# Optimization experiments

Measured on AMD Instinct MI355X. Metric: run time of the kernel, lower is better.

Reference implementation:

```python
import jax, jax.numpy as jnp
import numpy as np

L, C = 256, 20
BATCH = 1024


def _pairwise_mask(L, C, mask_type='pairwise'):
    # mask[l1, c1, l2, c2] nonzero iff positions interact (l2 - l1 >= 1, or == 1 for neighbor)
    ls = jnp.arange(L)
    d = ls[None, :] - ls[:, None]  # [L, L] = l2 - l1
    m = (d >= 1) if mask_type == 'pairwise' else (d == 1)
    return jnp.broadcast_to(m[:, None, :, None], (L, C, L, C)).astype(jnp.float32)


def setup_inputs() -> dict:
    key = jax.random.key(0)
    k1, k2, k3 = jax.random.split(key, 3)
    x_lc = jax.random.uniform(k1, (BATCH, L * C), dtype=jnp.float32)
    theta_0 = jnp.zeros((1,), dtype=jnp.float32)
    theta_lc = jax.random.normal(k2, (L, C), dtype=jnp.float32) / np.sqrt(L)
    theta_lclc = jax.random.normal(k3, (L, C, L, C), dtype=jnp.float32) / np.sqrt(L * L)
    return {"x_lc": x_lc, "theta_0": theta_0, "theta_lc": theta_lc, "theta_lclc": theta_lclc}


def reference(x_lc, theta_0, theta_lc, theta_lclc):
    Ld, Cd = theta_lc.shape
    mask = _pairwise_mask(Ld, Cd, 'pairwise')
    # additive term: sum_lc theta_lc * x_lc  -> [B, 1]
    lin = x_lc @ theta_lc.reshape(Ld * Cd)  # [B]
    # pairwise term: x^T (theta * mask) x, expressed as a masked GEMM instead of a
    # broadcasted [B, L, C, L, C] product
    Theta = (theta_lclc * mask).reshape(Ld * Cd, Ld * Cd)  # [LC, LC]
    xm = x_lc @ Theta  # [B, LC]
    quad = jnp.sum(xm * x_lc, axis=1)  # [B]
    phi = theta_0 + (lin + quad)[:, None]  # [B, 1]
    return phi
```

## Files before the change

### kernel.cpp

```cpp
#include <hip/hip_runtime.h>
#include <hip/hip_bf16.h>
#include <cstdint>
#include <cstddef>

#define LCN 5120
#define BN  1024
#define CN  20

typedef __attribute__((ext_vector_type(4))) float  floatx4;
typedef __attribute__((ext_vector_type(8))) short  shortx8;
typedef __attribute__((ext_vector_type(4))) unsigned short ushortx4;

static __device__ __forceinline__ unsigned short f2bf(float f) {
    __hip_bfloat16 h = __float2bfloat16(f);
    return *reinterpret_cast<unsigned short*>(&h);
}

static __device__ __forceinline__ void gload_lds16(const void* g, void* l) {
    __builtin_amdgcn_global_load_lds(
        (const __attribute__((address_space(1))) void*)g,
        (__attribute__((address_space(3))) void*)l,
        16, 0, 0);
}

__global__ __launch_bounds__(256) void k_conv(const float* __restrict__ th,
                                              unsigned short* __restrict__ Tn) {
    const int a  = blockIdx.y;
    const int t  = a >> 7;
    const int c0 = (CN * ((128 * t) / CN + 1)) / 512;
    const int bx = blockIdx.x;
    if (2 * (bx + 1) <= c0) return;
    const int kmin = CN * (a / CN + 1);
    const int col  = bx * 1024 + threadIdx.x * 4;
    const floatx4 v = *reinterpret_cast<const floatx4*>(th + (size_t)a * LCN + col);
    ushortx4 o;
#pragma unroll
    for (int e = 0; e < 4; ++e)
        o[e] = (col + e >= kmin) ? f2bf(v[e]) : (unsigned short)0;
    *reinterpret_cast<ushortx4*>(Tn + (size_t)a * LCN + col) = o;
}

__global__ __launch_bounds__(256) void k_init(const float* __restrict__ x,
                                              const float* __restrict__ th0,
                                              const float* __restrict__ thlc,
                                              float* __restrict__ out,
                                              unsigned short* __restrict__ Xb) {
    const int b = blockIdx.x;
    const int tid = threadIdx.x;
    const floatx4* xr = reinterpret_cast<const floatx4*>(x + (size_t)b * LCN);
    const floatx4* tr = reinterpret_cast<const floatx4*>(thlc);
    ushortx4* xw = reinterpret_cast<ushortx4*>(Xb + (size_t)b * LCN);
    float s = 0.0f;
    for (int k = tid; k < LCN / 4; k += 256) {
        const floatx4 a = xr[k], t2 = tr[k];
        s += a[0] * t2[0] + a[1] * t2[1] + a[2] * t2[2] + a[3] * t2[3];
        ushortx4 o;
#pragma unroll
        for (int e = 0; e < 4; ++e) o[e] = f2bf(a[e]);
        xw[k] = o;
    }
#pragma unroll
    for (int off = 32; off > 0; off >>= 1) s += __shfl_down(s, off, 64);
    __shared__ float ws4[4];
    if ((tid & 63) == 0) ws4[tid >> 6] = s;
    __syncthreads();
    if (tid == 0) out[b] = th0[0] + ws4[0] + ws4[1] + ws4[2] + ws4[3];
}

__global__ __launch_bounds__(256) void k_quad(
    const unsigned short* __restrict__ Xb,
    const unsigned short* __restrict__ Tn,
    float*                __restrict__ out,
    const int tot)
{
    const int bid  = blockIdx.x;
    const int xcd  = bid & 7;
    const int slot = bid >> 3;
    const int m    = slot & 7;
    const int g    = slot >> 3;
    int q = g * 8 + xcd;
    if (q >= tot) return;

    __shared__ unsigned short As[2][128 * 32];
    __shared__ unsigned short Bs[2][128 * 32];
    __shared__ float partial[128];

    const int tid  = threadIdx.x;
    const int lane = tid & 63;
    const int w    = tid >> 6;
    const int wm   = w & 1;
    const int wn   = w >> 1;
    const int lrow = lane & 15;
    const int kq   = lane >> 4;

    int n = 0, c = 0;
    for (int t = 0; t < 40; ++t) {
        const int c0t = (CN * ((128 * t) / CN + 1)) / 512;
        const int chn = 10 - c0t;
        if (q < chn) { n = t; c = c0t + q; break; }
        q -= chn;
    }
    const int b0 = m * 128;
    const int n0 = n * 128;
    const int k0 = c * 512;

    if (tid < 128) partial[tid] = 0.0f;

    floatx4 acc[4][4];
#pragma unroll
    for (int mt = 0; mt < 4; ++mt)
#pragma unroll
        for (int nt = 0; nt < 4; ++nt) acc[mt][nt] = (floatx4)0.0f;

    int grow[2], goff[2], loff[2];
#pragma unroll
    for (int t = 0; t < 2; ++t) {
        const int s    = t * 256 + tid;
        const int row  = s >> 2;
        const int gseg = ((s & 3) - (row >> 1)) & 3;
        grow[t] = row;
        goff[t] = gseg * 8;
        loff[t] = (t * 256 + w * 64) * 16;
    }
    int aoff[4], boff[4];
#pragma unroll
    for (int mt = 0; mt < 4; ++mt) {
        const int row = wm * 64 + mt * 16 + lrow;
        aoff[mt] = row * 32 + (((kq + (row >> 1)) & 3) << 3);
    }
#pragma unroll
    for (int nt = 0; nt < 4; ++nt) {
        const int row = wn * 64 + nt * 16 + lrow;
        boff[nt] = row * 32 + (((kq + (row >> 1)) & 3) << 3);
    }

#pragma unroll
    for (int t = 0; t < 2; ++t) {
        gload_lds16(Xb + (size_t)(b0 + grow[t]) * LCN + k0 + goff[t], (char*)As[0] + loff[t]);
        gload_lds16(Tn + (size_t)(n0 + grow[t]) * LCN + k0 + goff[t], (char*)Bs[0] + loff[t]);
    }

    for (int kk = 0; kk < 16; ++kk) {
        const int p = kk & 1;
        __syncthreads();
        if (kk < 15) {
            const int kc = k0 + (kk + 1) * 32;
#pragma unroll
            for (int t = 0; t < 2; ++t) {
                gload_lds16(Xb + (size_t)(b0 + grow[t]) * LCN + kc + goff[t], (char*)As[p ^ 1] + loff[t]);
                gload_lds16(Tn + (size_t)(n0 + grow[t]) * LCN + kc + goff[t], (char*)Bs[p ^ 1] + loff[t]);
            }
        }
        shortx8 af[4], bfr[4];
#pragma unroll
        for (int mt = 0; mt < 4; ++mt)
            af[mt] = *reinterpret_cast<const shortx8*>(As[p] + aoff[mt]);
#pragma unroll
        for (int nt = 0; nt < 4; ++nt)
            bfr[nt] = *reinterpret_cast<const shortx8*>(Bs[p] + boff[nt]);
#pragma unroll
        for (int mt = 0; mt < 4; ++mt)
#pragma unroll
            for (int nt = 0; nt < 4; ++nt)
                acc[mt][nt] = __builtin_amdgcn_mfma_f32_16x16x32_bf16(af[mt], bfr[nt], acc[mt][nt], 0, 0, 0);
    }

#pragma unroll
    for (int mt = 0; mt < 4; ++mt) {
#pragma unroll
        for (int r = 0; r < 4; ++r) {
            const int b = b0 + wm * 64 + mt * 16 + kq * 4 + r;
            float s = 0.0f;
#pragma unroll
            for (int nt = 0; nt < 4; ++nt) {
                const int a = n0 + wn * 64 + nt * 16 + lrow;
                const __hip_bfloat16 hv = *reinterpret_cast<const __hip_bfloat16*>(&Xb[(size_t)b * LCN + a]);
                s += acc[mt][nt][r] * __bfloat162float(hv);
            }
            s += __shfl_xor(s, 1, 64);
            s += __shfl_xor(s, 2, 64);
            s += __shfl_xor(s, 4, 64);
            s += __shfl_xor(s, 8, 64);
            if (lrow == 0) atomicAdd(&partial[b - b0], s);
        }
    }
    __syncthreads();
    if (tid < 128) atomicAdd(&out[b0 + tid], partial[tid]);
}

extern "C" void kernel_launch(void* const* d_in, const int* in_sizes, int n_in,
                              void* d_out, int out_size, void* d_ws, size_t ws_size,
                              hipStream_t stream) {
    const float* x      = (const float*)d_in[0];
    const float* th0    = (const float*)d_in[1];
    const float* thlc   = (const float*)d_in[2];
    const float* thlclc = (const float*)d_in[3];
    float* out = (float*)d_out;

    unsigned short* Tn = (unsigned short*)d_ws;
    unsigned short* Xb = (unsigned short*)((char*)d_ws + (size_t)LCN * LCN * 2);

    k_conv<<<dim3(LCN / 1024, LCN), 256, 0, stream>>>(thlclc, Tn);
    k_init<<<dim3(BN), 256, 0, stream>>>(x, th0, thlc, out, Xb);

    int tot = 0;
    for (int t = 0; t < 40; ++t) {
        const int c0t = (CN * ((128 * t) / CN + 1)) / 512;
        tot += 10 - c0t;
    }
    const int groups = (tot + 7) / 8;
    k_quad<<<dim3(groups * 64), 256, 0, stream>>>(Xb, Tn, out, tot);
}
```

Baseline: 232.1 us.

## Fuse theta bf16 conversion and masking into the GEMM B-tile load

Drops the separate conversion kernel that wrote a masked bf16 copy of theta to workspace. The quad kernel now reads fp32 theta directly into registers, applies the triangular mask, converts to bf16 and stores into LDS, with the next tile prefetched one step ahead. This saves a full pass over the large theta matrix and a kernel launch. In exchange each of the 8 batch-tile blocks re-reads fp32 theta, doubling the bytes per B tile and adding conversion ALU work and register pressure inside the GEMM loop.

```diff
diff --git a/kernel.cpp b/kernel.cpp
--- a/kernel.cpp
+++ b/kernel.cpp
@@ -10,6 +10,7 @@
 typedef __attribute__((ext_vector_type(4))) float  floatx4;
 typedef __attribute__((ext_vector_type(8))) short  shortx8;
 typedef __attribute__((ext_vector_type(4))) unsigned short ushortx4;
+typedef __attribute__((ext_vector_type(8))) unsigned short ushortx8;
 
 static __device__ __forceinline__ unsigned short f2bf(float f) {
     __hip_bfloat16 h = __float2bfloat16(f);
@@ -21,23 +22,6 @@
         (const __attribute__((address_space(1))) void*)g,
         (__attribute__((address_space(3))) void*)l,
         16, 0, 0);
-}
-
-__global__ __launch_bounds__(256) void k_conv(const float* __restrict__ th,
-                                              unsigned short* __restrict__ Tn) {
-    const int a  = blockIdx.y;
-    const int t  = a >> 7;
-    const int c0 = (CN * ((128 * t) / CN + 1)) / 512;
-    const int bx = blockIdx.x;
-    if (2 * (bx + 1) <= c0) return;
-    const int kmin = CN * (a / CN + 1);
-    const int col  = bx * 1024 + threadIdx.x * 4;
-    const floatx4 v = *reinterpret_cast<const floatx4*>(th + (size_t)a * LCN + col);
-    ushortx4 o;
-#pragma unroll
-    for (int e = 0; e < 4; ++e)
-        o[e] = (col + e >= kmin) ? f2bf(v[e]) : (unsigned short)0;
-    *reinterpret_cast<ushortx4*>(Tn + (size_t)a * LCN + col) = o;
 }
 
 __global__ __launch_bounds__(256) void k_init(const float* __restrict__ x,
@@ -69,7 +53,7 @@
 
 __global__ __launch_bounds__(256) void k_quad(
     const unsigned short* __restrict__ Xb,
-    const unsigned short* __restrict__ Tn,
+    const float*          __restrict__ Th,
     float*                __restrict__ out,
     const int tot)
 {
@@ -112,15 +96,17 @@
 #pragma unroll
         for (int nt = 0; nt < 4; ++nt) acc[mt][nt] = (floatx4)0.0f;
 
-    int grow[2], goff[2], loff[2];
+    int grow[2], goff[2], loffA[2], sbyte[2], kmin2[2];
 #pragma unroll
     for (int t = 0; t < 2; ++t) {
         const int s    = t * 256 + tid;
         const int row  = s >> 2;
         const int gseg = ((s & 3) - (row >> 1)) & 3;
-        grow[t] = row;
-        goff[t] = gseg * 8;
-        loff[t] = (t * 256 + w * 64) * 16;
+        grow[t]  = row;
+        goff[t]  = gseg * 8;
+        loffA[t] = (t * 256 + w * 64) * 16;
+        sbyte[t] = s * 16;
+        kmin2[t] = CN * ((n0 + row) / CN + 1);
     }
     int aoff[4], boff[4];
 #pragma unroll
@@ -134,22 +120,50 @@
         boff[nt] = row * 32 + (((kq + (row >> 1)) & 3) << 3);
     }
 
-#pragma unroll
-    for (int t = 0; t < 2; ++t) {
-        gload_lds16(Xb + (size_t)(b0 + grow[t]) * LCN + k0 + goff[t], (char*)As[0] + loff[t]);
-        gload_lds16(Tn + (size_t)(n0 + grow[t]) * LCN + k0 + goff[t], (char*)Bs[0] + loff[t]);
-    }
+    float br[2][8];
+
+#define LOAD_B(KC)                                                             \
+    {                                                                          \
+        _Pragma("unroll")                                                      \
+        for (int t = 0; t < 2; ++t) {                                          \
+            const float* gp = Th + (size_t)(n0 + grow[t]) * LCN + (KC) + goff[t]; \
+            const floatx4 v0 = *reinterpret_cast<const floatx4*>(gp);          \
+            const floatx4 v1 = *reinterpret_cast<const floatx4*>(gp + 4);      \
+            _Pragma("unroll")                                                  \
+            for (int e = 0; e < 4; ++e) { br[t][e] = v0[e]; br[t][e + 4] = v1[e]; } \
+        }                                                                      \
+    }
+
+#define CVT_WRITE_B(BUF, KC)                                                   \
+    {                                                                          \
+        _Pragma("unroll")                                                      \
+        for (int t = 0; t < 2; ++t) {                                          \
+            ushortx8 o;                                                        \
+            _Pragma("unroll")                                                  \
+            for (int e = 0; e < 8; ++e)                                        \
+                o[e] = ((KC) + goff[t] + e >= kmin2[t]) ? f2bf(br[t][e])       \
+                                                        : (unsigned short)0;  \
+            *reinterpret_cast<ushortx8*>((char*)Bs[BUF] + sbyte[t]) = o;       \
+        }                                                                      \
+    }
+
+#pragma unroll
+    for (int t = 0; t < 2; ++t)
+        gload_lds16(Xb + (size_t)(b0 + grow[t]) * LCN + k0 + goff[t], (char*)As[0] + loffA[t]);
+    LOAD_B(k0);
+    CVT_WRITE_B(0, k0);
+    LOAD_B(k0 + 32);
 
     for (int kk = 0; kk < 16; ++kk) {
         const int p = kk & 1;
         __syncthreads();
         if (kk < 15) {
-            const int kc = k0 + (kk + 1) * 32;
-#pragma unroll
-            for (int t = 0; t < 2; ++t) {
-                gload_lds16(Xb + (size_t)(b0 + grow[t]) * LCN + kc + goff[t], (char*)As[p ^ 1] + loff[t]);
-                gload_lds16(Tn + (size_t)(n0 + grow[t]) * LCN + kc + goff[t], (char*)Bs[p ^ 1] + loff[t]);
-            }
+            const int kcn = k0 + (kk + 1) * 32;
+#pragma unroll
+            for (int t = 0; t < 2; ++t)
+                gload_lds16(Xb + (size_t)(b0 + grow[t]) * LCN + kcn + goff[t], (char*)As[p ^ 1] + loffA[t]);
+            CVT_WRITE_B(p ^ 1, kcn);
+            if (kk < 14) LOAD_B(k0 + (kk + 2) * 32);
         }
         shortx8 af[4], bfr[4];
 #pragma unroll
@@ -186,6 +200,8 @@
     }
     __syncthreads();
     if (tid < 128) atomicAdd(&out[b0 + tid], partial[tid]);
+#undef LOAD_B
+#undef CVT_WRITE_B
 }
 
 extern "C" void kernel_launch(void* const* d_in, const int* in_sizes, int n_in,
@@ -197,10 +213,8 @@
     const float* thlclc = (const float*)d_in[3];
     float* out = (float*)d_out;
 
-    unsigned short* Tn = (unsigned short*)d_ws;
-    unsigned short* Xb = (unsigned short*)((char*)d_ws + (size_t)LCN * LCN * 2);
-
-    k_conv<<<dim3(LCN / 1024, LCN), 256, 0, stream>>>(thlclc, Tn);
+    unsigned short* Xb = (unsigned short*)d_ws;
+
     k_init<<<dim3(BN), 256, 0, stream>>>(x, th0, thlc, out, Xb);
 
     int tot = 0;
@@ -209,5 +223,5 @@
         tot += 10 - c0t;
     }
     const int groups = (tot + 7) / 8;
-    k_quad<<<dim3(groups * 64), 256, 0, stream>>>(Xb, Tn, out, tot);
-}
+    k_quad<<<dim3(groups * 64), 256, 0, stream>>>(Xb, thlclc, out, tot);
+}
```

Result: slower. 260.5 us (+12.2%).
